# Optimization experiments

Measured on AMD Instinct MI355X. Metric: run time of the kernel, lower is better.

Reference implementation:

```python
import jax, jax.numpy as jnp
import numpy as np

NUM_HIDDENS = 1024
NUM_VOCABS = 4096
BATCH = 64
SEQ = 256


def setup_inputs() -> dict:
    key = jax.random.key(0)
    ks = jax.random.split(key, 16)
    V, H = NUM_VOCABS, NUM_HIDDENS

    def gate(k1, k2):
        return (jax.random.normal(k1, (V, H), jnp.float32) * 0.01,
                jax.random.normal(k2, (H, H), jnp.float32) * 0.01,
                jnp.zeros((H,), jnp.float32))

    f_w_xh, f_w_hh, f_b = gate(ks[0], ks[1])
    i_w_xh, i_w_hh, i_b = gate(ks[2], ks[3])
    c_w_xh, c_w_hh, c_b = gate(ks[4], ks[5])
    o_w_xh, o_w_hh, o_b = gate(ks[6], ks[7])
    y_w_ho = jax.random.normal(ks[8], (H, V), jnp.float32) * 0.01
    y_b_o = jnp.zeros((V,), jnp.float32)
    inputs = jax.random.randint(ks[9], (BATCH, SEQ), 0, V, dtype=jnp.int64)
    H0 = jnp.zeros((BATCH, H), jnp.float32)
    C0 = jnp.zeros((BATCH, H), jnp.float32)
    return dict(inputs=inputs, H0=H0, C0=C0,
                f_w_xh=f_w_xh, f_w_hh=f_w_hh, f_b=f_b,
                i_w_xh=i_w_xh, i_w_hh=i_w_hh, i_b=i_b,
                c_w_xh=c_w_xh, c_w_hh=c_w_hh, c_b=c_b,
                o_w_xh=o_w_xh, o_w_hh=o_w_hh, o_b=o_b,
                y_w_ho=y_w_ho, y_b_o=y_b_o)


def reference(inputs, H0, C0,
              f_w_xh, f_w_hh, f_b,
              i_w_xh, i_w_hh, i_b,
              c_w_xh, c_w_hh, c_b,
              o_w_xh, o_w_hh, o_b,
              y_w_ho, y_b_o):
    # inputs: (batch, seq) int tokens -> iterate over time (seq, batch)
    tokens = inputs.T  # (T, B)

    def step(carry, x_t):
        Hs, Cs = carry
        # one_hot(x) @ W_xh == gather of rows: exact same math in fp32
        f = jax.nn.sigmoid(f_w_xh[x_t] + Hs @ f_w_hh + f_b)
        i = jax.nn.sigmoid(i_w_xh[x_t] + Hs @ i_w_hh + i_b)
        o = jax.nn.sigmoid(o_w_xh[x_t] + Hs @ o_w_hh + o_b)
        C_tilde = jnp.tanh(c_w_xh[x_t] + Hs @ c_w_hh + c_b)
        Cn = f * Cs + i * C_tilde
        Hn = o * Cn  # NOTE: source applies no tanh here (faithful)
        Y = Hn @ y_w_ho + y_b_o
        return (Hn, Cn), Y

    (Hf, Cf), Ys = jax.lax.scan(step, (H0, C0), tokens)
    return Ys, Hf, Cf  # Ys: (T, B, V)
```

## Files before the change

kernel.cpp:

```cpp
#include <hip/hip_runtime.h>
#include <stdint.h>
#include <stddef.h>


#define B_ 64
#define H_ 1024
#define V_ 4096
#define T_ 256
#define NWG 128

typedef __attribute__((ext_vector_type(8))) short short8;
typedef __attribute__((ext_vector_type(4))) float f32x4;
typedef __attribute__((ext_vector_type(4))) float float4_;
typedef __attribute__((ext_vector_type(4))) unsigned int uint4v;

static __device__ __forceinline__ unsigned short f2bf(float f) {
  union { float f; unsigned int u; } v; v.f = f;
  unsigned int u = v.u;
  unsigned int r = (u + 0x7fffu + ((u >> 16) & 1u)) >> 16;
  return (unsigned short)r;
}

static __device__ __forceinline__ void gload_lds16(const void* g, void* l) {
  __builtin_amdgcn_global_load_lds((const __attribute__((address_space(1))) unsigned int*)g,
                                   (__attribute__((address_space(3))) unsigned int*)l,
                                   16, 0, 0);
}

static __device__ __forceinline__ void poll8(unsigned int* cnt, unsigned int tgt, int lane) {
  bool ok = true;
  if (lane < 8)
    ok = __hip_atomic_load(cnt + 16 * lane, __ATOMIC_RELAXED, __HIP_MEMORY_SCOPE_AGENT) >= tgt;
  while (!__all(ok)) {
    if (lane < 8)
      ok = __hip_atomic_load(cnt + 16 * lane, __ATOMIC_RELAXED, __HIP_MEMORY_SCOPE_AGENT) >= tgt;
  }
  asm volatile("" ::: "memory");
  __builtin_amdgcn_sched_barrier(0);
}

__global__ void transpose_bf16_kernel(const float* __restrict__ src, int src_cols,
                                      unsigned short* __restrict__ dst,
                                      int c_mul, int c_add) {
  __shared__ float tile[64][65];
  const int k0 = blockIdx.x * 64, h0 = blockIdx.y * 64;
  const int t = threadIdx.x;
  {
    const int kk = t >> 2, seg = (t & 3) * 16;
    const float* s = src + (size_t)(k0 + kk) * src_cols + h0 + seg;
#pragma unroll
    for (int j = 0; j < 16; j += 4) {
      float4_ v = *(const float4_*)(s + j);
      tile[kk][seg + j + 0] = v[0];
      tile[kk][seg + j + 1] = v[1];
      tile[kk][seg + j + 2] = v[2];
      tile[kk][seg + j + 3] = v[3];
    }
  }
  __syncthreads();
  {
    const int hh = t >> 2, ks = (t & 3) * 16;
    const int c = (h0 + hh) * c_mul + c_add;
    short8 p0, p1;
#pragma unroll
    for (int j = 0; j < 8; ++j) {
      p0[j] = (short)f2bf(tile[ks + j][hh]);
      p1[j] = (short)f2bf(tile[ks + 8 + j][hh]);
    }
    unsigned short* d = dst + (size_t)c * 1024 + k0 + ks;
    *(short8*)(d) = p0;
    *(short8*)(d + 8) = p1;
  }
}

__global__ void init_kernel(const float* __restrict__ H0,
                            unsigned short* __restrict__ Hbuf0,
                            unsigned int* __restrict__ cnt) {
  const int i = blockIdx.x * 256 + threadIdx.x;
  Hbuf0[i] = f2bf(H0[i]);
  if (blockIdx.x == 0) cnt[threadIdx.x] = 0;
}

#define AOFF 65536

__launch_bounds__(256, 1)
__global__ void lstm_persistent_kernel(
    const unsigned short* __restrict__ Wcat,
    unsigned short* __restrict__ Hbuf,
    unsigned int* __restrict__ cnt,
    const float* __restrict__ C0,
    const float* __restrict__ xwf, const float* __restrict__ xwi,
    const float* __restrict__ xwc, const float* __restrict__ xwo,
    const float* __restrict__ bfv, const float* __restrict__ biv,
    const float* __restrict__ bcv, const float* __restrict__ bov,
    const int* __restrict__ tokens,
    float* __restrict__ outH, float* __restrict__ outC) {
  __shared__ __align__(16) unsigned char lds[147456];
  const int tid = threadIdx.x;
  const int wave = tid >> 6, lane = tid & 63;
  const int l15 = lane & 15, l4 = lane >> 4;
  const int wgc0 = blockIdx.x * 32;
  const int hbase0 = wgc0 >> 2;
  const int mychunk = blockIdx.x >> 4;
  const int brow = wave * 16 + l15;

  auto xw_of = [&](int g) -> const float* {
    return g == 0 ? xwf : g == 1 ? xwi : g == 2 ? xwc : xwo;
  };
  auto b_of = [&](int g) -> const float* {
    return g == 0 ? bfv : g == 1 ? biv : g == 2 ? bcv : bov;
  };

  int hL[2];
  float bias8[2][4], Creg[2], xg[2][4], xgn[2][4];
#pragma unroll
  for (int ni = 0; ni < 2; ++ni) {
    hL[ni] = hbase0 + ni * 4 + l4;
#pragma unroll
    for (int r = 0; r < 4; ++r) bias8[ni][r] = b_of(r)[hL[ni]];
    Creg[ni] = C0[(size_t)brow * 1024 + hL[ni]];
  }
  {
    const int tk = tokens[brow * T_ + 0];
#pragma unroll
    for (int ni = 0; ni < 2; ++ni)
#pragma unroll
      for (int r = 0; r < 4; ++r)
        xg[ni][r] = xw_of(r)[(size_t)tk * 1024 + hL[ni]];
  }

  {
    const char* Wb = (const char*)(Wcat + (size_t)wgc0 * 1024);
#pragma unroll
    for (int it = 0; it < 16; ++it) {
      const int D = it * 4096 + wave * 1024 + lane * 16;
      const int row = D >> 11, off = D & 2047;
      const int so = off ^ ((row & 7) << 4);
      gload_lds16(Wb + (size_t)row * 2048 + so, &lds[it * 4096 + wave * 1024]);
    }
  }
  asm volatile("s_waitcnt vmcnt(0)" ::: "memory");
  __syncthreads();

  auto stageA = [&](int buf, int c, const char* Hsrc) {
#pragma unroll
    for (int it2 = 0; it2 < 4; ++it2) {
      const int row = wave * 16 + it2 * 4 + l4;
      const int so = (l15 * 16) ^ ((row & 7) << 4);
      gload_lds16(Hsrc + (size_t)row * 2048 + c * 256 + so,
                  &lds[AOFF + buf * 16384 + wave * 4096 + it2 * 1024]);
    }
  };

  const int bswz = (l15 & 7) << 4;
  f32x4 acc[2];
  const f32x4 zz = {0.f, 0.f, 0.f, 0.f};

#pragma unroll 1
  for (int t = 0; t < T_; ++t) {
    if (t > 0) poll8(cnt, (unsigned int)(16 * t), lane);

    const char* Hs = (const char*)(Hbuf + (size_t)t * 65536);
    stageA(0, 0, Hs);
    stageA(1, 1, Hs);
    stageA(2, 2, Hs);
    stageA(3, 3, Hs);

    __builtin_amdgcn_sched_barrier(0);
    int tok2 = tokens[brow * T_ + ((t + 1) & (T_ - 1))];
    __builtin_amdgcn_sched_barrier(0);

    acc[0] = zz; acc[1] = zz;
#pragma unroll
    for (int c = 0; c < 8; ++c) {
      if (c < 4)       asm volatile("s_waitcnt vmcnt(13)" ::: "memory");
      else if (c == 4) asm volatile("s_waitcnt vmcnt(12)" ::: "memory");
      else if (c == 5) asm volatile("s_waitcnt vmcnt(8)" ::: "memory");
      else if (c == 6) asm volatile("s_waitcnt vmcnt(4)" ::: "memory");
      else             asm volatile("s_waitcnt vmcnt(0)" ::: "memory");
      __builtin_amdgcn_sched_barrier(0);
      if (c < 4) stageA((c + 4) % 5, c + 4, Hs);
      __builtin_amdgcn_sched_barrier(0);
      {
        const int abase = AOFF + (c % 5) * 16384;
        const int abyte = abase + brow * 256;
        const int aswz = (brow & 7) << 4;
#pragma unroll
        for (int ks = 0; ks < 4; ++ks) {
          const int koff = ks * 64 + l4 * 16;
          short8 a  = *(const short8*)&lds[abyte + (koff ^ aswz)];
          short8 b0 = *(const short8*)&lds[(size_t)l15 * 2048 + ((c * 256 + koff) ^ bswz)];
          short8 b1 = *(const short8*)&lds[(size_t)(16 + l15) * 2048 + ((c * 256 + koff) ^ bswz)];
          acc[0] = __builtin_amdgcn_mfma_f32_16x16x32_bf16(b0, a, acc[0], 0, 0, 0);
          acc[1] = __builtin_amdgcn_mfma_f32_16x16x32_bf16(b1, a, acc[1], 0, 0, 0);
        }
      }
      __builtin_amdgcn_sched_barrier(0);
    }

    if (t > 0) {
#pragma unroll
      for (int ni = 0; ni < 2; ++ni)
#pragma unroll
        for (int r = 0; r < 4; ++r) xg[ni][r] = xgn[ni][r];
    }

    unsigned short* Hout = Hbuf + (size_t)(t + 1) * 65536;
    unsigned int dat32[2][2];
#pragma unroll
    for (int ni = 0; ni < 2; ++ni) {
      const f32x4 v = acc[ni];
      const float pre0 = v[0] + xg[ni][0] + bias8[ni][0];
      const float pre1 = v[1] + xg[ni][1] + bias8[ni][1];
      const float pre2 = v[2] + xg[ni][2] + bias8[ni][2];
      const float pre3 = v[3] + xg[ni][3] + bias8[ni][3];
      const float pf = 1.f / (1.f + __expf(-pre0));
      const float pi = 1.f / (1.f + __expf(-pre1));
      const float e2 = __expf(2.f * pre2);
      const float pc = (e2 - 1.f) / (e2 + 1.f);
      const float po = 1.f / (1.f + __expf(-pre3));
      const float cn = pf * Creg[ni] + pi * pc;
      Creg[ni] = cn;
      const float hv = po * cn;
      const unsigned int sbf = f2bf(hv);
      const unsigned int p = sbf | (((unsigned int)__shfl_down(sbf, 16)) << 16);
      dat32[ni][0] = p;
      dat32[ni][1] = __shfl_down(p, 32);
      if (t == T_ - 1) {
        const size_t idx = (size_t)brow * 1024 + hL[ni];
        outH[idx] = hv; outC[idx] = cn;
      }
    }
    if (l4 == 0) {
      uint4v dat;
      dat.x = dat32[0][0]; dat.y = dat32[0][1];
      dat.z = dat32[1][0]; dat.w = dat32[1][1];
      const unsigned long long addr =
          (unsigned long long)(Hout + (size_t)brow * 1024 + hbase0);
      asm volatile("global_store_dwordx4 %0, %1, off sc0 sc1"
                   :: "v"(addr), "v"(dat) : "memory");
    }

    if (t < T_ - 1) {
      asm volatile("s_waitcnt vmcnt(0)" ::: "memory");
      __syncthreads();
      if (tid == 0)
        __hip_atomic_fetch_add(cnt + 16 * mychunk, 1u, __ATOMIC_RELAXED,
                               __HIP_MEMORY_SCOPE_AGENT);

#pragma unroll
      for (int ni = 0; ni < 2; ++ni)
#pragma unroll
        for (int r = 0; r < 4; ++r)
          xgn[ni][r] = xw_of(r)[(size_t)tok2 * 1024 + hL[ni]];
    }
  }
}

__launch_bounds__(256, 1)
__global__ void out_gemm_kernel(const unsigned short* __restrict__ A,
                                const unsigned short* __restrict__ Bw,
                                const float* __restrict__ bias,
                                float* __restrict__ Yout) {
  __shared__ unsigned char Ash[2][8192];
  __shared__ unsigned char Bsh[2][8192];
  const int tid = threadIdx.x;
  const int wave = tid >> 6, lane = tid & 63;
  const int wm = wave >> 1, wn = wave & 1;
  const int bid = blockIdx.x;
  const int tn = bid & 31, tm = bid >> 5;

  const char* Agb = (const char*)(A + (size_t)tm * 128 * 1024);
  const char* Bgb = (const char*)(Bw + (size_t)tn * 128 * 1024);

  f32x4 acc[4][4];
  const f32x4 zz = {0.f, 0.f, 0.f, 0.f};
#pragma unroll
  for (int mi = 0; mi < 4; ++mi)
#pragma unroll
    for (int ni = 0; ni < 4; ++ni) acc[mi][ni] = zz;

  auto stage = [&](int buf, int kc) {
#pragma unroll
    for (int j = 0; j < 2; ++j) {
      const int wbase = wave * 2048 + j * 1024;
      const int D = wbase + lane * 16;
      const int row = D >> 6, off = D & 63;
      const int so = off ^ ((row & 3) << 4);
      gload_lds16(Agb + (size_t)row * 2048 + kc * 64 + so, &Ash[buf][wbase]);
      gload_lds16(Bgb + (size_t)row * 2048 + kc * 64 + so, &Bsh[buf][wbase]);
    }
  };

  stage(0, 0);
  __syncthreads();

#pragma unroll 1
  for (int kc = 0; kc < 32; ++kc) {
    const int cur = kc & 1;
    if (kc < 31) stage(cur ^ 1, kc + 1);
    short8 a[4], b[4];
#pragma unroll
    for (int mi = 0; mi < 4; ++mi) {
      const int row = wm * 64 + mi * 16 + (lane & 15);
      const int off = ((lane >> 4) * 16) ^ ((row & 3) << 4);
      a[mi] = *(const short8*)&Ash[cur][row * 64 + off];
    }
#pragma unroll
    for (int ni = 0; ni < 4; ++ni) {
      const int row = wn * 64 + ni * 16 + (lane & 15);
      const int off = ((lane >> 4) * 16) ^ ((row & 3) << 4);
      b[ni] = *(const short8*)&Bsh[cur][row * 64 + off];
    }
#pragma unroll
    for (int mi = 0; mi < 4; ++mi)
#pragma unroll
      for (int ni = 0; ni < 4; ++ni)
        acc[mi][ni] = __builtin_amdgcn_mfma_f32_16x16x32_bf16(a[mi], b[ni], acc[mi][ni], 0, 0, 0);
    __syncthreads();
  }

  const int l15 = lane & 15, l4 = lane >> 4;
#pragma unroll
  for (int ni = 0; ni < 4; ++ni) {
    const int n = tn * 128 + wn * 64 + ni * 16 + l15;
    const float bv = bias[n];
#pragma unroll
    for (int mi = 0; mi < 4; ++mi) {
#pragma unroll
      for (int r = 0; r < 4; ++r) {
        const int m = tm * 128 + wm * 64 + mi * 16 + l4 * 4 + r;
        Yout[(size_t)m * 4096 + n] = acc[mi][ni][r] + bv;
      }
    }
  }
}

extern "C" void kernel_launch(void* const* d_in, const int* in_sizes, int n_in,
                              void* d_out, int out_size, void* d_ws, size_t ws_size,
                              hipStream_t stream) {
  const int* tokens   = (const int*)d_in[0];
  const float* H0     = (const float*)d_in[1];
  const float* C0     = (const float*)d_in[2];
  const float* f_w_xh = (const float*)d_in[3];
  const float* f_w_hh = (const float*)d_in[4];
  const float* f_b    = (const float*)d_in[5];
  const float* i_w_xh = (const float*)d_in[6];
  const float* i_w_hh = (const float*)d_in[7];
  const float* i_b    = (const float*)d_in[8];
  const float* c_w_xh = (const float*)d_in[9];
  const float* c_w_hh = (const float*)d_in[10];
  const float* c_b    = (const float*)d_in[11];
  const float* o_w_xh = (const float*)d_in[12];
  const float* o_w_hh = (const float*)d_in[13];
  const float* o_b    = (const float*)d_in[14];
  const float* y_w_ho = (const float*)d_in[15];
  const float* y_b_o  = (const float*)d_in[16];

  char* ws = (char*)d_ws;
  unsigned short* Wcat = (unsigned short*)ws;
  unsigned short* ywT  = (unsigned short*)(ws + (size_t)(8u << 20));
  unsigned short* Hbuf = (unsigned short*)(ws + (size_t)(16u << 20));
  unsigned int* cnt = (unsigned int*)(ws + (size_t)(16u << 20) + (size_t)257 * 65536 * 2);
  const size_t needed = (size_t)(16u << 20) + (size_t)257 * 65536 * 2 + 1024;
  if (ws_size < needed) return;

  const dim3 thr(256);
  hipLaunchKernelGGL(transpose_bf16_kernel, dim3(16, 16), thr, 0, stream, f_w_hh, 1024, Wcat, 4, 0);
  hipLaunchKernelGGL(transpose_bf16_kernel, dim3(16, 16), thr, 0, stream, i_w_hh, 1024, Wcat, 4, 1);
  hipLaunchKernelGGL(transpose_bf16_kernel, dim3(16, 16), thr, 0, stream, c_w_hh, 1024, Wcat, 4, 2);
  hipLaunchKernelGGL(transpose_bf16_kernel, dim3(16, 16), thr, 0, stream, o_w_hh, 1024, Wcat, 4, 3);
  hipLaunchKernelGGL(transpose_bf16_kernel, dim3(16, 64), thr, 0, stream, y_w_ho, 4096, ywT, 1, 0);
  hipLaunchKernelGGL(init_kernel, dim3(256), thr, 0, stream, H0, Hbuf, cnt);

  float* outH = (float*)d_out + (size_t)T_ * B_ * V_;
  hipLaunchKernelGGL(lstm_persistent_kernel, dim3(NWG), thr, 0, stream,
                     Wcat, Hbuf, cnt, C0,
                     f_w_xh, i_w_xh, c_w_xh, o_w_xh,
                     f_b, i_b, c_b, o_b,
                     tokens, outH, outH + 65536);

  hipLaunchKernelGGL(out_gemm_kernel, dim3(4096), thr, 0, stream,
                     Hbuf + 65536, ywT, y_b_o, (float*)d_out);
}
```

Baseline: 1.596 ms.

## Replace atomic chunk counters with per-wave flag array grid barrier

Each wave now writes its own step-number flag with a cache-bypassing store, so the per-step __syncthreads and atomic fetch_add on chunk counters go away. Waiters poll all 512 flags with two wide vector loads per lane and proceed once every flag has reached the step. This cuts serialization on contended atomic counters and the intra-block barrier in the recurrent loop, but each poll now reads more data and the code relies on sc0 sc1 stores being visible to other CUs.

```diff
diff --git a/kernel.cpp b/kernel.cpp
--- a/kernel.cpp
+++ b/kernel.cpp
@@ -27,13 +27,23 @@
                                    16, 0, 0);
 }
 
-static __device__ __forceinline__ void poll8(unsigned int* cnt, unsigned int tgt, int lane) {
-  bool ok = true;
-  if (lane < 8)
-    ok = __hip_atomic_load(cnt + 16 * lane, __ATOMIC_RELAXED, __HIP_MEMORY_SCOPE_AGENT) >= tgt;
-  while (!__all(ok)) {
-    if (lane < 8)
-      ok = __hip_atomic_load(cnt + 16 * lane, __ATOMIC_RELAXED, __HIP_MEMORY_SCOPE_AGENT) >= tgt;
+static __device__ __forceinline__ void sc_store_u32(unsigned int* p, unsigned int v) {
+  asm volatile("global_store_dword %0, %1, off sc0 sc1"
+               :: "v"((unsigned long long)p), "v"(v) : "memory");
+}
+
+static __device__ __forceinline__ void pollw(const unsigned int* arr, unsigned int tgt, int lane) {
+  const unsigned long long a0 = (unsigned long long)arr + (unsigned long long)lane * 16;
+  const unsigned long long a1 = a0 + 1024;
+  while (true) {
+    uint4v v0, v1;
+    asm volatile("global_load_dwordx4 %0, %2, off sc0 sc1\n\t"
+                 "global_load_dwordx4 %1, %3, off sc0 sc1\n\t"
+                 "s_waitcnt vmcnt(0)"
+                 : "=&v"(v0), "=&v"(v1) : "v"(a0), "v"(a1) : "memory");
+    const bool ok = v0[0] >= tgt && v0[1] >= tgt && v0[2] >= tgt && v0[3] >= tgt &&
+                    v1[0] >= tgt && v1[1] >= tgt && v1[2] >= tgt && v1[3] >= tgt;
+    if (__all(ok)) break;
   }
   asm volatile("" ::: "memory");
   __builtin_amdgcn_sched_barrier(0);
@@ -75,10 +85,10 @@
 
 __global__ void init_kernel(const float* __restrict__ H0,
                             unsigned short* __restrict__ Hbuf0,
-                            unsigned int* __restrict__ cnt) {
+                            unsigned int* __restrict__ arr) {
   const int i = blockIdx.x * 256 + threadIdx.x;
   Hbuf0[i] = f2bf(H0[i]);
-  if (blockIdx.x == 0) cnt[threadIdx.x] = 0;
+  if (i < 512) sc_store_u32(arr + i, 0u);
 }
 
 #define AOFF 65536
@@ -87,7 +97,7 @@
 __global__ void lstm_persistent_kernel(
     const unsigned short* __restrict__ Wcat,
     unsigned short* __restrict__ Hbuf,
-    unsigned int* __restrict__ cnt,
+    unsigned int* __restrict__ arr,
     const float* __restrict__ C0,
     const float* __restrict__ xwf, const float* __restrict__ xwi,
     const float* __restrict__ xwc, const float* __restrict__ xwo,
@@ -101,8 +111,8 @@
   const int l15 = lane & 15, l4 = lane >> 4;
   const int wgc0 = blockIdx.x * 32;
   const int hbase0 = wgc0 >> 2;
-  const int mychunk = blockIdx.x >> 4;
   const int brow = wave * 16 + l15;
+  unsigned int* myslot = arr + blockIdx.x * 4 + wave;
 
   auto xw_of = [&](int g) -> const float* {
     return g == 0 ? xwf : g == 1 ? xwi : g == 2 ? xwc : xwo;
@@ -158,7 +168,7 @@
 
 #pragma unroll 1
   for (int t = 0; t < T_; ++t) {
-    if (t > 0) poll8(cnt, (unsigned int)(16 * t), lane);
+    if (t > 0) pollw(arr, (unsigned int)t, lane);
 
     const char* Hs = (const char*)(Hbuf + (size_t)t * 65536);
     stageA(0, 0, Hs);
@@ -243,10 +253,7 @@
 
     if (t < T_ - 1) {
       asm volatile("s_waitcnt vmcnt(0)" ::: "memory");
-      __syncthreads();
-      if (tid == 0)
-        __hip_atomic_fetch_add(cnt + 16 * mychunk, 1u, __ATOMIC_RELAXED,
-                               __HIP_MEMORY_SCOPE_AGENT);
+      if (lane == 0) sc_store_u32(myslot, (unsigned int)(t + 1));
 
 #pragma unroll
       for (int ni = 0; ni < 2; ++ni)
@@ -361,8 +368,8 @@
   unsigned short* Wcat = (unsigned short*)ws;
   unsigned short* ywT  = (unsigned short*)(ws + (size_t)(8u << 20));
   unsigned short* Hbuf = (unsigned short*)(ws + (size_t)(16u << 20));
-  unsigned int* cnt = (unsigned int*)(ws + (size_t)(16u << 20) + (size_t)257 * 65536 * 2);
-  const size_t needed = (size_t)(16u << 20) + (size_t)257 * 65536 * 2 + 1024;
+  unsigned int* arr = (unsigned int*)(ws + (size_t)(16u << 20) + (size_t)257 * 65536 * 2);
+  const size_t needed = (size_t)(16u << 20) + (size_t)257 * 65536 * 2 + 2048;
   if (ws_size < needed) return;
 
   const dim3 thr(256);
@@ -371,11 +378,11 @@
   hipLaunchKernelGGL(transpose_bf16_kernel, dim3(16, 16), thr, 0, stream, c_w_hh, 1024, Wcat, 4, 2);
   hipLaunchKernelGGL(transpose_bf16_kernel, dim3(16, 16), thr, 0, stream, o_w_hh, 1024, Wcat, 4, 3);
   hipLaunchKernelGGL(transpose_bf16_kernel, dim3(16, 64), thr, 0, stream, y_w_ho, 4096, ywT, 1, 0);
-  hipLaunchKernelGGL(init_kernel, dim3(256), thr, 0, stream, H0, Hbuf, cnt);
+  hipLaunchKernelGGL(init_kernel, dim3(256), thr, 0, stream, H0, Hbuf, arr);
 
   float* outH = (float*)d_out + (size_t)T_ * B_ * V_;
   hipLaunchKernelGGL(lstm_persistent_kernel, dim3(NWG), thr, 0, stream,
-                     Wcat, Hbuf, cnt, C0,
+                     Wcat, Hbuf, arr, C0,
                      f_w_xh, i_w_xh, c_w_xh, o_w_xh,
                      f_b, i_b, c_b, o_b,
                      tokens, outH, outH + 65536);
```

New measurement: 1.347 ms. -15.6%, faster.
